# Performance work log

Measured on AMD Instinct MI355X. Metric: run time of the kernel, lower is better.

Reference implementation:

```python
import jax, jax.numpy as jnp
import numpy as np
import math

LOG2PI = math.log(2.0 * math.pi)


def _pair_sum(m1, v1, m2, v2, w):
    """sum_{i,j} w[i,j] * exp(delta_ij) for diagonal 2-D Gaussians.

    m1,v1: [K1,2] means / diagonal variances; m2,v2: [K2,2]; w: [K1,K2].
    Closed form of the torch code's 2x2 inverse/det/mm chain exploiting the
    fact that all covariances are diagonal (cov = diag((wh/2)^2)).
    """
    ci = 1.0 / v1[:, None, :]                      # [K1,1,2] = cov_inv_i diag
    cj = 1.0 / v2[None, :, :]                      # [1,K2,2] = cov_inv_j diag
    s = ci + cj                                    # [K1,K2,2] = cov_inv_ij diag
    mij = (m1[:, None, :] * ci + m2[None, :, :] * cj) / s   # combined mean
    quad = (jnp.sum(mij * mij * s, -1)
            - jnp.sum(m1 * m1 / v1, -1)[:, None]
            - jnp.sum(m2 * m2 / v2, -1)[None, :])            # [K1,K2]
    # log(det(cov_inv_ij) / (det(cov_inv_i) * det(cov_inv_j)))
    logdet = (jnp.sum(jnp.log(s), -1)
              + jnp.sum(jnp.log(v1), -1)[:, None]
              + jnp.sum(jnp.log(v2), -1)[None, :])           # [K1,K2]
    delta = 0.5 * (quad - logdet - 2.0 * LOG2PI)   # x_dim = 2
    return jnp.sum(w * jnp.exp(delta))


def _cs_div(p_m, p_v, p_a, q_m, q_v, q_a):
    pq = _pair_sum(p_m, p_v, q_m, q_v, p_a @ q_a.T)
    pp = _pair_sum(p_m, p_v, p_m, p_v, p_a @ p_a.T)
    qq = _pair_sum(q_m, q_v, q_m, q_v, q_a @ q_a.T)
    return 2.0 * jnp.log(pq) - jnp.log(pp) - jnp.log(qq)


def _forward(pred_bboxes, pred_labels, gt_bboxes, gt_labels):
    num_classes = pred_labels.shape[2] - 1
    pred_alpha = (jax.nn.sigmoid(pred_labels[:, :, -1])[:, :, None]
                  * jax.nn.softmax(pred_labels[:, :, :-1], axis=2))   # [bs,kp,C]
    gt_alpha = jax.nn.one_hot(gt_labels, num_classes, dtype=pred_alpha.dtype)
    pred_m = pred_bboxes[:, :, :2]
    pred_v = jnp.square(pred_bboxes[:, :, 2:] / 2.0)
    gt_m = gt_bboxes[:, :, :2]
    gt_v = jnp.square(gt_bboxes[:, :, 2:] / 2.0)
    per_img = jax.vmap(_cs_div)(gt_m, gt_v, gt_alpha, pred_m, pred_v, pred_alpha)
    return -jnp.sum(per_img)


def setup_inputs() -> dict:
    key = jax.random.key(0)
    k1, k2, k3, k4 = jax.random.split(key, 4)
    BS, KP, KG, NC = 32, 1000, 100, 80
    # widths/heights must be strictly positive -> uniform in [0.05, 1)
    pred_bboxes = jax.random.uniform(k1, (BS, KP, 4), jnp.float32, 0.05, 1.0)
    pred_labels = jax.random.normal(k2, (BS, KP, NC + 1), jnp.float32)
    gt_bboxes = jax.random.uniform(k3, (BS, KG, 4), jnp.float32, 0.05, 1.0)
    gt_labels = jax.random.randint(k4, (BS, KG), 0, NC)
    return {"pred_bboxes": pred_bboxes, "pred_labels": pred_labels,
            "gt_bboxes": gt_bboxes, "gt_labels": gt_labels}


def reference(pred_bboxes, pred_labels, gt_bboxes, gt_labels):
    return _forward(pred_bboxes, pred_labels, gt_bboxes, gt_labels)
```

## Files before the change

kernel.cpp:

```cpp
#include <hip/hip_runtime.h>
#include <math.h>

#define BS 32
#define KP 1000
#define KPP 1024
#define KG 100
#define NC 80
#define SK 96
#define LP 104
#define NT 8
#define NPAIR 36
#define NQQ (BS * NPAIR)
#define NPPQ (5 * BS)
#define NALL (NQQ + NPPQ)
#define NPERIMG 41
#define GCNT 512

using bf16x8 = __attribute__((ext_vector_type(8))) short;
using f32x4  = __attribute__((ext_vector_type(4))) float;
using f32x2  = __attribute__((ext_vector_type(2))) float;

__device__ __forceinline__ float wave_reduce_sum(float v) {
#pragma unroll
    for (int m = 32; m > 0; m >>= 1) v += __shfl_xor(v, m, 64);
    return v;
}
__device__ __forceinline__ float wave_reduce_max(float v) {
#pragma unroll
    for (int m = 32; m > 0; m >>= 1) v = fmaxf(v, __shfl_xor(v, m, 64));
    return v;
}

__device__ __forceinline__ unsigned short f2bf(float f) {
    unsigned int u = __float_as_uint(f);
    u += 0x7fffu + ((u >> 16) & 1u);
    return (unsigned short)(u >> 16);
}
__device__ __forceinline__ float bf2f(unsigned short h) {
    return __uint_as_float(((unsigned int)h) << 16);
}

__device__ __forceinline__ float kval(float4 a, float4 b) {
    f32x2 S = (f32x2){a.z, a.w} + (f32x2){b.z, b.w};
    f32x2 d = (f32x2){a.x, a.y} - (f32x2){b.x, b.y};
    f32x2 d2 = d * d;
    f32x2 t = d2 * S.yx;
    float num = t.x + t.y;
    float P = S.x * S.y;
    float rs = __builtin_amdgcn_rsqf(P);
    float q = num * rs * rs;
    return 0.15915494309189535f * rs * __expf(-0.5f * q);
}

__global__ __launch_bounds__(256) void alpha_kernel(const float* __restrict__ pl,
                                                    unsigned short* __restrict__ ah,
                                                    float* __restrict__ acc) {
    if (blockIdx.x == 0) {
#pragma unroll
        for (int k = 0; k < 3; ++k) acc[threadIdx.x + 256 * k] = 0.0f;
    }
    int wave = threadIdx.x >> 6;
    int lane = threadIdx.x & 63;
    int rr = blockIdx.x * 4 + wave;
    int b = rr >> 10, r = rr & (KPP - 1);
    unsigned short* oh = ah + (size_t)rr * SK;
    if (r < KP) {
        const float* x = pl + ((size_t)b * KP + r) * (NC + 1);
        float l0 = x[lane];
        float l1 = (lane < 16) ? x[64 + lane] : -1e30f;
        float obj = x[NC];
        float m = wave_reduce_max(fmaxf(l0, l1));
        float e0 = __expf(l0 - m);
        float e1 = (lane < 16) ? __expf(l1 - m) : 0.0f;
        float s = wave_reduce_sum(e0 + e1);
        float sig = 1.0f / (1.0f + __expf(-obj));
        float sc = sig / s;
        oh[lane] = f2bf(e0 * sc);
        if (lane < 32) oh[64 + lane] = (lane < 16) ? f2bf(e1 * sc) : 0;
    } else {
        oh[lane] = 0;
        if (lane < 32) oh[64 + lane] = 0;
    }
}

__global__ __launch_bounds__(256, 3) void main_kernel(const float* __restrict__ pb,
                                                      const unsigned short* __restrict__ ahg,
                                                      const float* __restrict__ gtb,
                                                      const int* __restrict__ gtl,
                                                      float* __restrict__ acc,
                                                      float* __restrict__ out) {
    __shared__ short lds[2 * 128 * LP];
    __shared__ float red[4];
    __shared__ int last;

    int tid = threadIdx.x;
    int lane = tid & 63, w = tid >> 6;
    int bi = blockIdx.x;
    int b;

    if (bi < NQQ) {
        short* la = lds;
        short* lbb = lds + 128 * LP;
        int qi = bi;
        b = qi & 31;
        int t = qi >> 5;
        int it = 0, rem = t;
        while (rem >= NT - it) { rem -= NT - it; ++it; }
        int jt = it + rem;
        int i0 = it * 128, j0 = jt * 128;

        {
            int side = tid >> 7, r = tid & 127;
            int gi = (side ? j0 : i0) + r;
            float4 v = make_float4(0.0f, 0.0f, 1.0f, 1.0f);
            if (gi < KP) {
                float4 x = ((const float4*)pb)[b * KP + gi];
                v = make_float4(x.x, x.y, 0.25f * x.z * x.z, 0.25f * x.w * x.w);
            }
            short* L = side ? lbb : la;
            *(float4*)(L + r * LP + 96) = v;
        }

        {
            const float4* sa = (const float4*)(ahg + ((size_t)(b << 10) + i0) * SK);
#pragma unroll
            for (int k = 0; k < 6; ++k) {
                int o = tid + k * 256;
                int row = o / 12, slot = o - row * 12;
                *(float4*)(la + row * LP + slot * 8) = sa[o];
            }
            if (jt != it) {
                const float4* sb = (const float4*)(ahg + ((size_t)(b << 10) + j0) * SK);
#pragma unroll
                for (int k = 0; k < 6; ++k) {
                    int o = tid + k * 256;
                    int row = o / 12, slot = o - row * 12;
                    *(float4*)(lbb + row * LP + slot * 8) = sb[o];
                }
            }
        }
        __syncthreads();
        const short* LB = (jt != it) ? lbb : la;

        int wy = w >> 1, wx = w & 1;
        int m15 = lane & 15, quad = lane >> 4;
        int ar = wy * 64 + m15;
        int br = wx * 64 + m15;

        f32x4 c4[4][4];
#pragma unroll
        for (int r = 0; r < 4; ++r)
#pragma unroll
            for (int s = 0; s < 4; ++s) c4[r][s] = (f32x4){0.0f, 0.0f, 0.0f, 0.0f};

#pragma unroll
        for (int ks = 0; ks < 3; ++ks) {
            int kk = ks * 32 + quad * 8;
            bf16x8 bh[4];
#pragma unroll
            for (int cg = 0; cg < 4; ++cg)
                bh[cg] = *(const bf16x8*)(LB + (br + cg * 16) * LP + kk);
#pragma unroll
            for (int rg = 0; rg < 4; ++rg) {
                bf16x8 xh = *(const bf16x8*)(la + (ar + rg * 16) * LP + kk);
#pragma unroll
                for (int cg = 0; cg < 4; ++cg)
                    c4[rg][cg] = __builtin_amdgcn_mfma_f32_16x16x32_bf16(xh, bh[cg], c4[rg][cg], 0, 0, 0);
            }
        }

        float4 pj[4];
        int jb = wx * 64 + m15;
#pragma unroll
        for (int cg = 0; cg < 4; ++cg)
            pj[cg] = *(const float4*)(lbb + (jb + cg * 16) * LP + 96);
        float part = 0.0f;
        int ib = wy * 64 + quad * 4;
#pragma unroll
        for (int rg = 0; rg < 4; ++rg) {
#pragma unroll
            for (int e = 0; e < 4; ++e) {
                float4 pi = *(const float4*)(la + (ib + rg * 16 + e) * LP + 96);
#pragma unroll
                for (int cg = 0; cg < 4; ++cg)
                    part += c4[rg][cg][e] * kval(pi, pj[cg]);
            }
        }
        if (jt != it) part *= 2.0f;

        part = wave_reduce_sum(part);
        if (lane == 0) red[w] = part;
        __syncthreads();
        if (tid == 0)
            atomicAdd(&acc[b * 16 + 2], red[0] + red[1] + red[2] + red[3]);
    } else {
        int pi = bi - NQQ;
        b = pi & 31;
        int p5 = pi >> 5;
        short* lalpha = lds;
        float4* gm = (float4*)(lds + 24576);
        int* gl = (int*)(lds + 24576 + 800);
        if (tid < KG) {
            float4 x = ((const float4*)gtb)[b * KG + tid];
            gm[tid] = make_float4(x.x, x.y, 0.25f * x.z * x.z, 0.25f * x.w * x.w);
            gl[tid] = gtl[b * KG + tid];
        }
        if (p5 < 4) {
            const float4* sa = (const float4*)(ahg + ((size_t)(b << 10) + p5 * 256) * SK);
#pragma unroll
            for (int k = 0; k < 12; ++k) {
                int o = tid + k * 256;
                *(float4*)(lalpha + o * 8) = sa[o];
            }
        }
        __syncthreads();
        float part = 0.0f;
        if (p5 < 4) {
            int j = p5 * 256 + tid;
            if (j < KP) {
                float4 x = ((const float4*)pb)[b * KP + j];
                float4 pm = make_float4(x.x, x.y, 0.25f * x.z * x.z, 0.25f * x.w * x.w);
                const unsigned short* arow = (const unsigned short*)lalpha + tid * SK;
#pragma unroll 4
                for (int i = 0; i < KG; ++i) {
                    part += bf2f(arow[gl[i]]) * kval(gm[i], pm);
                }
            }
        } else {
            for (int p = tid; p < KG * KG; p += 256) {
                int i = p / KG;
                int j = p - i * KG;
                if (gl[i] == gl[j]) part += kval(gm[i], gm[j]);
            }
        }
        part = wave_reduce_sum(part);
        if (lane == 0) red[w] = part;
        __syncthreads();
        if (tid == 0) {
            float s = red[0] + red[1] + red[2] + red[3];
            atomicAdd(&acc[b * 16 + ((p5 < 4) ? 0 : 1)], s);
        }
    }

    if (tid == 0) {
        __threadfence();
        unsigned int o = atomicAdd((unsigned int*)(acc + b * 16 + 4), 1u);
        int l = 0;
        if (o == NPERIMG - 1) {
            __threadfence();
            unsigned int g = atomicAdd((unsigned int*)(acc + GCNT), 1u);
            l = (g == BS - 1) ? 1 : 0;
        }
        last = l;
    }
    __syncthreads();
    if (last && tid < 64) {
        float v = 0.0f;
        if (tid < BS) {
            float pq = atomicAdd(&acc[tid * 16 + 0], 0.0f);
            float pp = atomicAdd(&acc[tid * 16 + 1], 0.0f);
            float qq = atomicAdd(&acc[tid * 16 + 2], 0.0f);
            v = 2.0f * logf(pq) - logf(pp) - logf(qq);
        }
        v = wave_reduce_sum(v);
        if (tid == 0) out[0] = -v;
    }
}

extern "C" void kernel_launch(void* const* d_in, const int* in_sizes, int n_in,
                              void* d_out, int out_size, void* d_ws, size_t ws_size,
                              hipStream_t stream) {
    (void)in_sizes; (void)n_in; (void)out_size; (void)ws_size;
    const float* pred_bb  = (const float*)d_in[0];
    const float* pred_lab = (const float*)d_in[1];
    const float* gt_bb    = (const float*)d_in[2];
    const int*   gt_lab   = (const int*)d_in[3];
    float* out = (float*)d_out;

    unsigned short* ah = (unsigned short*)d_ws;
    float* acc = (float*)(ah + (size_t)BS * KPP * SK);

    hipLaunchKernelGGL(alpha_kernel, dim3(BS * KPP / 4), dim3(256), 0, stream,
                       pred_lab, ah, acc);
    hipLaunchKernelGGL(main_kernel, dim3(NALL), dim3(256), 0, stream,
                       pred_bb, ah, gt_bb, gt_lab, acc, out);
}
```

Measured before the change: 105.3 us.

## Loop each QQ block over several j-tiles reusing the loaded i-tile

Each pred-pred block now keeps its i-tile in LDS and loops over every other j-tile (split into two halves), instead of one block per (i,j) tile pair. This reuses the A tile and cuts the number of blocks and atomics. In exchange, per-block work is serialized with extra syncs, the loads are not double-buffered, and the halves are unevenly loaded, which lowers parallelism and increases tail imbalance.

```diff
diff --git a/kernel.cpp b/kernel.cpp
--- a/kernel.cpp
+++ b/kernel.cpp
@@ -9,11 +9,11 @@
 #define SK 96
 #define LP 104
 #define NT 8
-#define NPAIR 36
-#define NQQ (BS * NPAIR)
+#define NIT 15
+#define NQQ (BS * NIT)
 #define NPPQ (5 * BS)
 #define NALL (NQQ + NPPQ)
-#define NPERIMG 41
+#define NPERIMG 20
 #define GCNT 512
 
 using bf16x8 = __attribute__((ext_vector_type(8))) short;
@@ -100,27 +100,21 @@
 
     if (bi < NQQ) {
         short* la = lds;
-        short* lbb = lds + 128 * LP;
-        int qi = bi;
-        b = qi & 31;
-        int t = qi >> 5;
-        int it = 0, rem = t;
-        while (rem >= NT - it) { rem -= NT - it; ++it; }
-        int jt = it + rem;
-        int i0 = it * 128, j0 = jt * 128;
-
-        {
-            int side = tid >> 7, r = tid & 127;
-            int gi = (side ? j0 : i0) + r;
+        short* lb = lds + 128 * LP;
+        b = bi & 31;
+        int p = bi >> 5;
+        int it = p >> 1, half = p & 1;
+        int i0 = it * 128;
+
+        if (tid < 128) {
+            int gi = i0 + tid;
             float4 v = make_float4(0.0f, 0.0f, 1.0f, 1.0f);
             if (gi < KP) {
                 float4 x = ((const float4*)pb)[b * KP + gi];
                 v = make_float4(x.x, x.y, 0.25f * x.z * x.z, 0.25f * x.w * x.w);
             }
-            short* L = side ? lbb : la;
-            *(float4*)(L + r * LP + 96) = v;
-        }
-
+            *(float4*)(la + tid * LP + 96) = v;
+        }
         {
             const float4* sa = (const float4*)(ahg + ((size_t)(b << 10) + i0) * SK);
 #pragma unroll
@@ -129,64 +123,80 @@
                 int row = o / 12, slot = o - row * 12;
                 *(float4*)(la + row * LP + slot * 8) = sa[o];
             }
-            if (jt != it) {
-                const float4* sb = (const float4*)(ahg + ((size_t)(b << 10) + j0) * SK);
-#pragma unroll
-                for (int k = 0; k < 6; ++k) {
-                    int o = tid + k * 256;
-                    int row = o / 12, slot = o - row * 12;
-                    *(float4*)(lbb + row * LP + slot * 8) = sb[o];
-                }
-            }
-        }
-        __syncthreads();
-        const short* LB = (jt != it) ? lbb : la;
+        }
 
         int wy = w >> 1, wx = w & 1;
         int m15 = lane & 15, quad = lane >> 4;
         int ar = wy * 64 + m15;
         int br = wx * 64 + m15;
-
-        f32x4 c4[4][4];
-#pragma unroll
-        for (int r = 0; r < 4; ++r)
-#pragma unroll
-            for (int s = 0; s < 4; ++s) c4[r][s] = (f32x4){0.0f, 0.0f, 0.0f, 0.0f};
-
-#pragma unroll
-        for (int ks = 0; ks < 3; ++ks) {
-            int kk = ks * 32 + quad * 8;
-            bf16x8 bh[4];
+        int jb = wx * 64 + m15;
+        int ib = wy * 64 + quad * 4;
+
+        float part = 0.0f;
+        bool first = true;
+        for (int jt = it + half; jt < NT; jt += 2) {
+            int j0 = jt * 128;
+            if (!first) __syncthreads();
+            if (tid < 128) {
+                int gi = j0 + tid;
+                float4 v = make_float4(0.0f, 0.0f, 1.0f, 1.0f);
+                if (gi < KP) {
+                    float4 x = ((const float4*)pb)[b * KP + gi];
+                    v = make_float4(x.x, x.y, 0.25f * x.z * x.z, 0.25f * x.w * x.w);
+                }
+                *(float4*)(lb + tid * LP + 96) = v;
+            }
+            {
+                const float4* sb = (const float4*)(ahg + ((size_t)(b << 10) + j0) * SK);
+#pragma unroll
+                for (int k = 0; k < 6; ++k) {
+                    int o = tid + k * 256;
+                    int row = o / 12, slot = o - row * 12;
+                    *(float4*)(lb + row * LP + slot * 8) = sb[o];
+                }
+            }
+            __syncthreads();
+
+            f32x4 c4[4][4];
+#pragma unroll
+            for (int r = 0; r < 4; ++r)
+#pragma unroll
+                for (int s = 0; s < 4; ++s) c4[r][s] = (f32x4){0.0f, 0.0f, 0.0f, 0.0f};
+
+#pragma unroll
+            for (int ks = 0; ks < 3; ++ks) {
+                int kk = ks * 32 + quad * 8;
+                bf16x8 bh[4];
+#pragma unroll
+                for (int cg = 0; cg < 4; ++cg)
+                    bh[cg] = *(const bf16x8*)(lb + (br + cg * 16) * LP + kk);
+#pragma unroll
+                for (int rg = 0; rg < 4; ++rg) {
+                    bf16x8 xh = *(const bf16x8*)(la + (ar + rg * 16) * LP + kk);
+#pragma unroll
+                    for (int cg = 0; cg < 4; ++cg)
+                        c4[rg][cg] = __builtin_amdgcn_mfma_f32_16x16x32_bf16(xh, bh[cg], c4[rg][cg], 0, 0, 0);
+                }
+            }
+
+            float4 pj[4];
 #pragma unroll
             for (int cg = 0; cg < 4; ++cg)
-                bh[cg] = *(const bf16x8*)(LB + (br + cg * 16) * LP + kk);
+                pj[cg] = *(const float4*)(lb + (jb + cg * 16) * LP + 96);
+            float tpart = 0.0f;
 #pragma unroll
             for (int rg = 0; rg < 4; ++rg) {
-                bf16x8 xh = *(const bf16x8*)(la + (ar + rg * 16) * LP + kk);
-#pragma unroll
-                for (int cg = 0; cg < 4; ++cg)
-                    c4[rg][cg] = __builtin_amdgcn_mfma_f32_16x16x32_bf16(xh, bh[cg], c4[rg][cg], 0, 0, 0);
-            }
-        }
-
-        float4 pj[4];
-        int jb = wx * 64 + m15;
-#pragma unroll
-        for (int cg = 0; cg < 4; ++cg)
-            pj[cg] = *(const float4*)(lbb + (jb + cg * 16) * LP + 96);
-        float part = 0.0f;
-        int ib = wy * 64 + quad * 4;
-#pragma unroll
-        for (int rg = 0; rg < 4; ++rg) {
-#pragma unroll
-            for (int e = 0; e < 4; ++e) {
-                float4 pi = *(const float4*)(la + (ib + rg * 16 + e) * LP + 96);
-#pragma unroll
-                for (int cg = 0; cg < 4; ++cg)
-                    part += c4[rg][cg][e] * kval(pi, pj[cg]);
-            }
-        }
-        if (jt != it) part *= 2.0f;
+#pragma unroll
+                for (int e = 0; e < 4; ++e) {
+                    float4 pi = *(const float4*)(la + (ib + rg * 16 + e) * LP + 96);
+#pragma unroll
+                    for (int cg = 0; cg < 4; ++cg)
+                        tpart += c4[rg][cg][e] * kval(pi, pj[cg]);
+                }
+            }
+            part += (jt != it) ? 2.0f * tpart : tpart;
+            first = false;
+        }
 
         part = wave_reduce_sum(part);
         if (lane == 0) red[w] = part;
```

After: 99.25 us, median of 2. 5.8% less time.
